# Optimization experiments

Measured on AMD Instinct MI355X. Metric: run time of the kernel, lower is better.

The kernel has to match this reference:

```python
import jax, jax.numpy as jnp
import numpy as np

B, T, V, D, U = 256, 1024, 6, 64, 64  # batch, seq, vocab, embed dim, lstm units


def _lstm_dir(x_seq, mask_seq, Wk, Wr, b, reverse):
    # x_seq: [B,T,D], mask_seq: [B,T] bool. Keras gate order: i, f, g(cell), o.
    Bc, Tc, _ = x_seq.shape
    Uc = Wr.shape[0]
    if reverse:
        x_seq = x_seq[:, ::-1, :]
        mask_seq = mask_seq[:, ::-1]
    # precompute input projections for all timesteps (one big GEMM)
    xproj = jnp.einsum('btd,dg->tbg', x_seq, Wk) + b          # [T,B,4U]
    m = jnp.swapaxes(mask_seq, 0, 1)[..., None]               # [T,B,1]

    def step(carry, inp):
        h, c = carry
        xp, mt = inp
        z = xp + h @ Wr                                        # [B,4U]
        i, f, g, o = jnp.split(z, 4, axis=-1)
        i = jax.nn.sigmoid(i)
        f = jax.nn.sigmoid(f)
        g = jnp.tanh(g)
        o = jax.nn.sigmoid(o)
        c_new = f * c + i * g
        h_new = o * jnp.tanh(c_new)
        # masked steps carry state through and repeat previous output
        h = jnp.where(mt, h_new, h)
        c = jnp.where(mt, c_new, c)
        return (h, c), h

    h0 = jnp.zeros((Bc, Uc), x_seq.dtype)
    _, ys = jax.lax.scan(step, (h0, h0), (xproj, m))           # ys: [T,B,U]
    ys = jnp.swapaxes(ys, 0, 1)                                # [B,T,U]
    if reverse:
        ys = ys[:, ::-1, :]
    return ys


def reference(tokens, emb, Wk_f, Wr_f, b_f, Wk_b, Wr_b, b_b, Wd, bd):
    x = emb[tokens]                                            # [B,T,D]
    mask = jnp.any(x != 0, axis=-1)                            # Masking(0): all-zero feature vec -> masked
    y_f = _lstm_dir(x, mask, Wk_f, Wr_f, b_f, reverse=False)   # [B,T,U]
    y_b = _lstm_dir(x, mask, Wk_b, Wr_b, b_b, reverse=True)    # [B,T,U]
    y = jnp.concatenate([y_f, y_b], axis=-1)                   # [B,T,2U]
    last = y[:, -1, :]                                         # [B,2U]
    return last @ Wd + bd                                      # [B,1]


def setup_inputs() -> dict:
    key = jax.random.key(0)
    ks = jax.random.split(key, 8)
    return {
        'tokens': jax.random.randint(ks[0], (B, T), 0, V, dtype=jnp.int32),
        'emb': jax.random.normal(ks[1], (V, D), dtype=jnp.float32),
        'Wk_f': jax.random.normal(ks[2], (D, 4 * U), dtype=jnp.float32) * 0.05,
        'Wr_f': jax.random.normal(ks[3], (U, 4 * U), dtype=jnp.float32) * 0.05,
        'b_f': jnp.zeros((4 * U,), dtype=jnp.float32),
        'Wk_b': jax.random.normal(ks[4], (D, 4 * U), dtype=jnp.float32) * 0.05,
        'Wr_b': jax.random.normal(ks[5], (U, 4 * U), dtype=jnp.float32) * 0.05,
        'b_b': jnp.zeros((4 * U,), dtype=jnp.float32),
        'Wd': jax.random.normal(ks[6], (2 * U, 1), dtype=jnp.float32) * 0.05,
        'bd': jnp.zeros((1,), dtype=jnp.float32),
    }
```

## Files before the change

kernel.cpp:

```cpp
#include <hip/hip_runtime.h>


constexpr int kB = 256;
constexpr int kT = 1024;
constexpr int kV = 6;
constexpr int kD = 64;
constexpr int kU = 64;
constexpr int kG = 256;

__device__ __forceinline__ float fast_rcp(float x) { return __builtin_amdgcn_rcpf(x); }
__device__ __forceinline__ float sig_f(float z)  { return fast_rcp(1.0f + __expf(-z)); }
__device__ __forceinline__ float tanh_f(float z) { return 2.0f * fast_rcp(1.0f + __expf(-2.0f * z)) - 1.0f; }

template <int CTRL>
__device__ __forceinline__ float dpp_addq(float x) {
    const int y = __builtin_amdgcn_mov_dpp(__float_as_int(x), CTRL, 0xF, 0xF, true);
    return x + __int_as_float(y);
}
constexpr int kXor1 = 0xB1;
constexpr int kXor2 = 0x4E;

__global__ __launch_bounds__(256, 1) void bilstm_last_kernel(
    const int*   __restrict__ tokens,
    const float* __restrict__ emb,
    const float* __restrict__ Wk_f,
    const float* __restrict__ Wr_f,
    const float* __restrict__ b_f,
    const float* __restrict__ Wk_b,
    const float* __restrict__ b_b,
    const float* __restrict__ Wd,
    const float* __restrict__ bd,
    float*       __restrict__ out)
{
    __shared__ float s_emb[kV * kD];
    __shared__ float s_projP[kV * kG];
    __shared__ int   s_tok[kT];
    __shared__ float __align__(16) s_h[2][kU];
    __shared__ float s_act[kG];

    const int b   = blockIdx.x;
    const int tid = threadIdx.x;
    const int l   = tid & 63;
    const int wv  = tid >> 6;
    const int s   = l & 3;
    const int k   = l >> 2;
    const int u   = wv * 16 + k;

    for (int i = tid; i < kV * kD; i += 256) s_emb[i] = emb[i];
    ((int4*)s_tok)[tid] = ((const int4*)(tokens + b * kT))[tid];
    if (tid < kU) { s_h[0][tid] = 0.0f; s_h[1][tid] = 0.0f; }
    __syncthreads();

    unsigned int mb = 0;
#pragma unroll
    for (int v = 0; v < kV; ++v) {
        const unsigned long long bb = __ballot(s_emb[v * kD + l] != 0.0f);
        mb |= (bb != 0ull) ? (1u << v) : 0u;
    }

    const int tokL = s_tok[kT - 1];

    float a0 = b_f[tid], a1 = a0, a2 = a0, a3 = a0, a4 = a0, a5 = a0;
    float accb = b_b[tid];
    for (int d = 0; d < kD; ++d) {
        const float wkf = Wk_f[d * kG + tid];
        const float wkb = Wk_b[d * kG + tid];
        a0 = fmaf(s_emb[0 * kD + d], wkf, a0);
        a1 = fmaf(s_emb[1 * kD + d], wkf, a1);
        a2 = fmaf(s_emb[2 * kD + d], wkf, a2);
        a3 = fmaf(s_emb[3 * kD + d], wkf, a3);
        a4 = fmaf(s_emb[4 * kD + d], wkf, a4);
        a5 = fmaf(s_emb[5 * kD + d], wkf, a5);
        accb = fmaf(s_emb[tokL * kD + d], wkb, accb);
    }
    {
        const int g0 = tid >> 6, u0 = tid & 63, w0 = u0 >> 4, k0 = u0 & 15;
        const int q = w0 * 64 + k0 * 4 + g0;
        s_projP[0 * kG + q] = a0;
        s_projP[1 * kG + q] = a1;
        s_projP[2 * kG + q] = a2;
        s_projP[3 * kG + q] = a3;
        s_projP[4 * kG + q] = a4;
        s_projP[5 * kG + q] = a5;
    }

    float ab;
    if (tid < 128)      ab = sig_f(accb);
    else if (tid < 192) ab = tanh_f(accb);
    else                ab = sig_f(accb);
    s_act[tid] = ab;
    __syncthreads();
    float hb_val = 0.0f;
    if (tid < kU) {
        const float cb = s_act[tid] * s_act[2 * kU + tid];
        const float hb = s_act[3 * kU + tid] * tanh_f(cb);
        hb_val = ((mb >> tokL) & 1) ? hb : 0.0f;
    }

#define DECLW(g, jb)                                                  \
    float4 wq##g##_##jb;                                              \
    wq##g##_##jb.x = Wr_f[(16 * s + 4 * jb + 0) * kG + (g * 64 + u)]; \
    wq##g##_##jb.y = Wr_f[(16 * s + 4 * jb + 1) * kG + (g * 64 + u)]; \
    wq##g##_##jb.z = Wr_f[(16 * s + 4 * jb + 2) * kG + (g * 64 + u)]; \
    wq##g##_##jb.w = Wr_f[(16 * s + 4 * jb + 3) * kG + (g * 64 + u)];
    DECLW(0,0) DECLW(0,1) DECLW(0,2) DECLW(0,3)
    DECLW(1,0) DECLW(1,1) DECLW(1,2) DECLW(1,3)
    DECLW(2,0) DECLW(2,1) DECLW(2,2) DECLW(2,3)
    DECLW(3,0) DECLW(3,1) DECLW(3,2) DECLW(3,3)
#undef DECLW

    float c = 0.0f, hreg = 0.0f;
    __syncthreads();

    const int tok0 = s_tok[0];
    float zcur = s_projP[tok0 * kG + tid];
    int   msk  = (mb >> tok0) & 1;
    int   tokA = s_tok[1];

    for (int t = 0; t < kT; ++t) {
        const int rp = t & 1, wp = rp ^ 1;

        const float znext = s_projP[tokA * kG + tid];
        const int   mskn  = (mb >> tokA) & 1;
        const int   tokB  = s_tok[(t + 2) & (kT - 1)];

        const float4* hp = (const float4*)s_h[rp];
        const float4 hv0 = hp[s * 4 + 0];
        const float4 hv1 = hp[s * 4 + 1];
        const float4 hv2 = hp[s * 4 + 2];
        const float4 hv3 = hp[s * 4 + 3];

        float p0 = (s == 0) ? zcur : 0.0f;
        float p1 = (s == 1) ? zcur : 0.0f;
        float p2 = (s == 2) ? zcur : 0.0f;
        float p3 = (s == 3) ? zcur : 0.0f;
#define MACQ(g, jb)                                  \
        p##g = fmaf(hv##jb.x, wq##g##_##jb.x, p##g); \
        p##g = fmaf(hv##jb.y, wq##g##_##jb.y, p##g); \
        p##g = fmaf(hv##jb.z, wq##g##_##jb.z, p##g); \
        p##g = fmaf(hv##jb.w, wq##g##_##jb.w, p##g);
        MACQ(0,0) MACQ(1,0) MACQ(2,0) MACQ(3,0)
        MACQ(0,1) MACQ(1,1) MACQ(2,1) MACQ(3,1)
        MACQ(0,2) MACQ(1,2) MACQ(2,2) MACQ(3,2)
        MACQ(0,3) MACQ(1,3) MACQ(2,3) MACQ(3,3)
#undef MACQ

        p0 = dpp_addq<kXor1>(p0); p1 = dpp_addq<kXor1>(p1);
        p2 = dpp_addq<kXor1>(p2); p3 = dpp_addq<kXor1>(p3);
        p0 = dpp_addq<kXor2>(p0); p1 = dpp_addq<kXor2>(p1);
        p2 = dpp_addq<kXor2>(p2); p3 = dpp_addq<kXor2>(p3);

        const float ai = sig_f(p0);
        const float af = sig_f(p1);
        const float ag = tanh_f(p2);
        const float ao = sig_f(p3);
        const float cn = fmaf(af, c, ai * ag);
        const float hn = ao * tanh_f(cn);
        if (msk) { c = cn; hreg = hn; }

        if (s == 0) s_h[wp][u] = hreg;
        __syncthreads();

        zcur = znext; msk = mskn; tokA = tokB;
    }

    if (tid < kU) {
        float v = s_h[0][tid] * Wd[tid] + hb_val * Wd[kU + tid];
#pragma unroll
        for (int off = 32; off > 0; off >>= 1) v += __shfl_down(v, off, 64);
        if (tid == 0) out[b] = v + bd[0];
    }
}

extern "C" void kernel_launch(void* const* d_in, const int* in_sizes, int n_in,
                              void* d_out, int out_size, void* d_ws, size_t ws_size,
                              hipStream_t stream) {
    const int*   tokens = (const int*)d_in[0];
    const float* emb    = (const float*)d_in[1];
    const float* Wk_f   = (const float*)d_in[2];
    const float* Wr_f   = (const float*)d_in[3];
    const float* b_f    = (const float*)d_in[4];
    const float* Wk_b   = (const float*)d_in[5];
    const float* b_b    = (const float*)d_in[7];
    const float* Wd     = (const float*)d_in[8];
    const float* bd     = (const float*)d_in[9];
    float* out = (float*)d_out;

    bilstm_last_kernel<<<kB, 256, 0, stream>>>(
        tokens, emb, Wk_f, Wr_f, b_f, Wk_b, b_b, Wd, bd, out);
}
```

Baseline: 429.4 us.

## Distribute gate activations across quad lanes and unroll recurrence loop by two

```diff
diff --git a/kernel.cpp b/kernel.cpp
--- a/kernel.cpp
+++ b/kernel.cpp
@@ -8,17 +8,21 @@
 constexpr int kU = 64;
 constexpr int kG = 256;
 
-__device__ __forceinline__ float fast_rcp(float x) { return __builtin_amdgcn_rcpf(x); }
-__device__ __forceinline__ float sig_f(float z)  { return fast_rcp(1.0f + __expf(-z)); }
-__device__ __forceinline__ float tanh_f(float z) { return 2.0f * fast_rcp(1.0f + __expf(-2.0f * z)) - 1.0f; }
+#define LOG2E 1.44269504f
 
 template <int CTRL>
-__device__ __forceinline__ float dpp_addq(float x) {
-    const int y = __builtin_amdgcn_mov_dpp(__float_as_int(x), CTRL, 0xF, 0xF, true);
-    return x + __int_as_float(y);
+__device__ __forceinline__ float dppf(float x) {
+    return __int_as_float(
+        __builtin_amdgcn_mov_dpp(__float_as_int(x), CTRL, 0xF, 0xF, true));
 }
 constexpr int kXor1 = 0xB1;
 constexpr int kXor2 = 0x4E;
+constexpr int kB0 = 0x00, kB1 = 0x55, kB2 = 0xAA, kB3 = 0xFF;
+
+__device__ __forceinline__ float fast_rcp(float x) { return __builtin_amdgcn_rcpf(x); }
+__device__ __forceinline__ float exp2_f(float x)   { return __builtin_amdgcn_exp2f(x); }
+__device__ __forceinline__ float sig_f(float z)  { return fast_rcp(1.0f + exp2_f(-LOG2E * z)); }
+__device__ __forceinline__ float tanh_f(float z) { return 2.0f * fast_rcp(1.0f + exp2_f(-2.0f * LOG2E * z)) - 1.0f; }
 
 __global__ __launch_bounds__(256, 1) void bilstm_last_kernel(
     const int*   __restrict__ tokens,
@@ -51,12 +55,13 @@
     if (tid < kU) { s_h[0][tid] = 0.0f; s_h[1][tid] = 0.0f; }
     __syncthreads();
 
-    unsigned int mb = 0;
+    unsigned int mbv = 0;
 #pragma unroll
     for (int v = 0; v < kV; ++v) {
         const unsigned long long bb = __ballot(s_emb[v * kD + l] != 0.0f);
-        mb |= (bb != 0ull) ? (1u << v) : 0u;
-    }
+        mbv |= (bb != 0ull) ? (1u << v) : 0u;
+    }
+    const unsigned int smb = __builtin_amdgcn_readfirstlane(mbv);
 
     const int tokL = s_tok[kT - 1];
 
@@ -94,7 +99,7 @@
     if (tid < kU) {
         const float cb = s_act[tid] * s_act[2 * kU + tid];
         const float hb = s_act[3 * kU + tid] * tanh_f(cb);
-        hb_val = ((mb >> tokL) & 1) ? hb : 0.0f;
+        hb_val = ((smb >> tokL) & 1) ? hb : 0.0f;
     }
 
 #define DECLW(g, jb)                                                  \
@@ -109,60 +114,71 @@
     DECLW(3,0) DECLW(3,1) DECLW(3,2) DECLW(3,3)
 #undef DECLW
 
+    const bool  isg    = (s == 2);
+    const float aScale = isg ? -2.0f * LOG2E : -LOG2E;
+    const float aMul   = isg ? 2.0f : 1.0f;
+    const float aAdd   = isg ? -1.0f : 0.0f;
+
     float c = 0.0f, hreg = 0.0f;
     __syncthreads();
 
-    const int tok0 = s_tok[0];
-    float zcur = s_projP[tok0 * kG + tid];
-    int   msk  = (mb >> tok0) & 1;
-    int   tokA = s_tok[1];
-
-    for (int t = 0; t < kT; ++t) {
-        const int rp = t & 1, wp = rp ^ 1;
-
-        const float znext = s_projP[tokA * kG + tid];
-        const int   mskn  = (mb >> tokA) & 1;
-        const int   tokB  = s_tok[(t + 2) & (kT - 1)];
-
-        const float4* hp = (const float4*)s_h[rp];
-        const float4 hv0 = hp[s * 4 + 0];
-        const float4 hv1 = hp[s * 4 + 1];
-        const float4 hv2 = hp[s * 4 + 2];
-        const float4 hv3 = hp[s * 4 + 3];
-
-        float p0 = (s == 0) ? zcur : 0.0f;
-        float p1 = (s == 1) ? zcur : 0.0f;
-        float p2 = (s == 2) ? zcur : 0.0f;
-        float p3 = (s == 3) ? zcur : 0.0f;
+    int stok0 = __builtin_amdgcn_readfirstlane(s_tok[0]);
+    float zcur = s_projP[stok0 * kG + tid];
+    int   mskc = (smb >> stok0) & 1;
+    int   stokA = __builtin_amdgcn_readfirstlane(s_tok[1]);
+
+#define STEP(RP, WP, TT)                                                      \
+    {                                                                         \
+        const int   vtokB = s_tok[((TT) + 2) & (kT - 1)];                     \
+        const float znext = s_projP[stokA * kG + tid];                        \
+        const int   mskn  = (int)((smb >> stokA) & 1);                        \
+        const float4* hp = (const float4*)s_h[RP];                            \
+        const float4 hv0 = hp[s * 4 + 0];                                     \
+        const float4 hv1 = hp[s * 4 + 1];                                     \
+        const float4 hv2 = hp[s * 4 + 2];                                     \
+        const float4 hv3 = hp[s * 4 + 3];                                     \
+        float p0 = 0.0f, p1 = 0.0f, p2 = 0.0f, p3 = 0.0f;                     \
+        MACQ(0,0) MACQ(1,0) MACQ(2,0) MACQ(3,0)                               \
+        MACQ(0,1) MACQ(1,1) MACQ(2,1) MACQ(3,1)                               \
+        MACQ(0,2) MACQ(1,2) MACQ(2,2) MACQ(3,2)                               \
+        MACQ(0,3) MACQ(1,3) MACQ(2,3) MACQ(3,3)                               \
+                         \
+        p0 += dppf<kXor1>(p0); p1 += dppf<kXor1>(p1);                         \
+        p2 += dppf<kXor1>(p2); p3 += dppf<kXor1>(p3);                         \
+        \
+        float X = (s & 1) ? p1 : p0;                                          \
+        float Y = (s & 1) ? p3 : p2;                                          \
+        X += dppf<kXor2>(X); Y += dppf<kXor2>(Y);                             \
+        const float z = ((s & 2) ? Y : X) + zcur;                             \
+                                      \
+        const float e = exp2_f(z * aScale);                                   \
+        const float r = fast_rcp(1.0f + e);                                   \
+        const float a = fmaf(r, aMul, aAdd);                                  \
+                     \
+        const float ai = dppf<kB0>(a);                                        \
+        const float af = dppf<kB1>(a);                                        \
+        const float ag = dppf<kB2>(a);                                        \
+        const float ao = dppf<kB3>(a);                                        \
+        const float cn = fmaf(af, c, ai * ag);                                \
+        const float hn = ao * tanh_f(cn);                                     \
+        if (mskc) { c = cn; hreg = hn; }                  \
+        if (s == 0) s_h[WP][u] = hreg;                                        \
+        __syncthreads();                                                      \
+        zcur = znext; mskc = mskn; stokA = __builtin_amdgcn_readfirstlane(vtokB); \
+    }
+
 #define MACQ(g, jb)                                  \
         p##g = fmaf(hv##jb.x, wq##g##_##jb.x, p##g); \
         p##g = fmaf(hv##jb.y, wq##g##_##jb.y, p##g); \
         p##g = fmaf(hv##jb.z, wq##g##_##jb.z, p##g); \
         p##g = fmaf(hv##jb.w, wq##g##_##jb.w, p##g);
-        MACQ(0,0) MACQ(1,0) MACQ(2,0) MACQ(3,0)
-        MACQ(0,1) MACQ(1,1) MACQ(2,1) MACQ(3,1)
-        MACQ(0,2) MACQ(1,2) MACQ(2,2) MACQ(3,2)
-        MACQ(0,3) MACQ(1,3) MACQ(2,3) MACQ(3,3)
+
+    for (int t = 0; t < kT; t += 2) {
+        STEP(0, 1, t)
+        STEP(1, 0, t + 1)
+    }
 #undef MACQ
-
-        p0 = dpp_addq<kXor1>(p0); p1 = dpp_addq<kXor1>(p1);
-        p2 = dpp_addq<kXor1>(p2); p3 = dpp_addq<kXor1>(p3);
-        p0 = dpp_addq<kXor2>(p0); p1 = dpp_addq<kXor2>(p1);
-        p2 = dpp_addq<kXor2>(p2); p3 = dpp_addq<kXor2>(p3);
-
-        const float ai = sig_f(p0);
-        const float af = sig_f(p1);
-        const float ag = tanh_f(p2);
-        const float ao = sig_f(p3);
-        const float cn = fmaf(af, c, ai * ag);
-        const float hn = ao * tanh_f(cn);
-        if (msk) { c = cn; hreg = hn; }
-
-        if (s == 0) s_h[wp][u] = hreg;
-        __syncthreads();
-
-        zcur = znext; msk = mskn; tokA = tokB;
-    }
+#undef STEP
 
     if (tid < kU) {
         float v = s_h[0][tid] * Wd[tid] + hb_val * Wd[kU + tid];
```

Measured after the change: 391.6 us. -8.8%, faster.
